# Optimization experiments

Measured on AMD Instinct MI355X. Metric: run time of the kernel, lower is better.

Reference implementation:

```python
import jax, jax.numpy as jnp
import numpy as np

N = 100000      # nodes
E = 1600000     # edges (avg degree 16)
D = 64          # feature dim


def setup_inputs() -> dict:
    key = jax.random.key(0)
    k1, k2, k3, k4 = jax.random.split(key, 4)
    x = jax.random.normal(k1, (N, D), dtype=jnp.float32)
    indices = jax.random.randint(k2, (E,), 0, N, dtype=jnp.int64)
    # valid CSR indptr: sorted, starts at 0, ends at E
    inner = jnp.sort(jax.random.randint(k3, (N - 1,), 0, E, dtype=jnp.int64))
    indptr = jnp.concatenate([
        jnp.zeros((1,), dtype=jnp.int64),
        inner,
        jnp.full((1,), E, dtype=jnp.int64),
    ])
    values = jax.random.normal(k4, (E,), dtype=jnp.float32)
    return {"x": x, "indptr": indptr, "indices": indices, "values": values}


def reference(x, indptr, indices, values):
    # CSR SpMM: out[i] = sum_{k in [indptr[i], indptr[i+1])} values[k] * x[indices[k]]
    num_edges = indices.shape[0]
    num_nodes = indptr.shape[0] - 1
    # recover row id of each edge from indptr (CSR row decompression)
    row = jnp.searchsorted(indptr, jnp.arange(num_edges, dtype=indptr.dtype), side='right') - 1
    gathered = values[:, None] * x[indices]            # [E, D] irregular gather
    out = jax.ops.segment_sum(gathered, row, num_segments=num_nodes)  # [N, D]
    return out
```

## Files before the change

kernel.cpp:

```cpp
#include <hip/hip_runtime.h>

#define DIM 64

__global__ __launch_bounds__(256) void spmm_quad_kernel(
    const float* __restrict__ x,
    const int*   __restrict__ indptr,
    const int*   __restrict__ indices,
    const float* __restrict__ values,
    float*       __restrict__ out,
    int n_nodes)
{
    const int row  = (int)((blockIdx.x * blockDim.x + threadIdx.x) >> 6);
    const int lane = (int)(threadIdx.x & 63);
    if (row >= n_nodes) return;

    const int start = indptr[row];
    const int end   = indptr[row + 1];
    const int g     = lane >> 4;
    const unsigned col4 = (unsigned)(lane & 15) << 2;

    float ax = 0.f, ay = 0.f, az = 0.f, aw = 0.f;

    if (start < end) {
        const int last = end - 1;
        for (int k = start; k < end; k += 16) {
            const int e0 = k +  0 + g;
            const int e1 = k +  4 + g;
            const int e2 = k +  8 + g;
            const int e3 = k + 12 + g;
            const int ce0 = e0 <= last ? e0 : last;
            const int ce1 = e1 <= last ? e1 : last;
            const int ce2 = e2 <= last ? e2 : last;
            const int ce3 = e3 <= last ? e3 : last;

            const int c0 = indices[ce0];
            const int c1 = indices[ce1];
            const int c2 = indices[ce2];
            const int c3 = indices[ce3];
            const float w0 = (e0 <= last) ? values[ce0] : 0.0f;
            const float w1 = (e1 <= last) ? values[ce1] : 0.0f;
            const float w2 = (e2 <= last) ? values[ce2] : 0.0f;
            const float w3 = (e3 <= last) ? values[ce3] : 0.0f;

            const float4 a0 = *(const float4*)(x + (((unsigned)c0) << 6) + col4);
            const float4 a1 = *(const float4*)(x + (((unsigned)c1) << 6) + col4);
            const float4 a2 = *(const float4*)(x + (((unsigned)c2) << 6) + col4);
            const float4 a3 = *(const float4*)(x + (((unsigned)c3) << 6) + col4);

            ax += w0 * a0.x; ay += w0 * a0.y; az += w0 * a0.z; aw += w0 * a0.w;
            ax += w1 * a1.x; ay += w1 * a1.y; az += w1 * a1.z; aw += w1 * a1.w;
            ax += w2 * a2.x; ay += w2 * a2.y; az += w2 * a2.z; aw += w2 * a2.w;
            ax += w3 * a3.x; ay += w3 * a3.y; az += w3 * a3.z; aw += w3 * a3.w;
        }
    }

    ax += __shfl_xor(ax, 16); ay += __shfl_xor(ay, 16);
    az += __shfl_xor(az, 16); aw += __shfl_xor(aw, 16);
    ax += __shfl_xor(ax, 32); ay += __shfl_xor(ay, 32);
    az += __shfl_xor(az, 32); aw += __shfl_xor(aw, 32);

    if (lane < 16) {
        float4 r; r.x = ax; r.y = ay; r.z = az; r.w = aw;
        *(float4*)(out + ((size_t)row << 6) + col4) = r;
    }
}

extern "C" void kernel_launch(void* const* d_in, const int* in_sizes, int n_in,
                              void* d_out, int out_size, void* d_ws, size_t ws_size,
                              hipStream_t stream) {
    const float* x       = (const float*)d_in[0];
    const int*   indptr  = (const int*)  d_in[1];
    const int*   indices = (const int*)  d_in[2];
    const float* values  = (const float*)d_in[3];
    float*       out     = (float*)d_out;

    const int n_nodes = in_sizes[1] - 1;

    const int threads = 256;
    const int rows_per_block = threads / 64;
    const int blocks = (n_nodes + rows_per_block - 1) / rows_per_block;

    spmm_quad_kernel<<<blocks, threads, 0, stream>>>(
        x, indptr, indices, values, out, n_nodes);
}
```

Baseline: 61.75 us.

## Convert x to fp16 in workspace and gather half-precision rows in SpMM

Adds a pre-pass kernel that converts the dense feature matrix to fp16 in the workspace. A new SpMM kernel then gathers 128-byte half rows with 8 lanes per edge and 8 edges per wave-step, accumulating in fp32. The aim is to halve the bytes moved by the irregular gather, at the cost of an extra conversion pass over x each call and a loss of precision in the inputs. If the workspace is too small it falls back to the original fp32 kernel.

```diff
diff --git a/kernel.cpp b/kernel.cpp
--- a/kernel.cpp
+++ b/kernel.cpp
@@ -1,6 +1,83 @@
 #include <hip/hip_runtime.h>
+#include <hip/hip_fp16.h>
 
 #define DIM 64
+
+__global__ __launch_bounds__(256) void cvt_half_kernel(
+    const float* __restrict__ x, __half* __restrict__ xh, int n4)
+{
+    int i = blockIdx.x * blockDim.x + threadIdx.x;
+    const int stride = gridDim.x * blockDim.x;
+    for (; i < n4; i += stride) {
+        const float4 v = ((const float4*)x)[i];
+        __half2 h0 = __floats2half2_rn(v.x, v.y);
+        __half2 h1 = __floats2half2_rn(v.z, v.w);
+        uint2 u;
+        u.x = *(const unsigned int*)&h0;
+        u.y = *(const unsigned int*)&h1;
+        ((uint2*)xh)[i] = u;
+    }
+}
+
+__global__ __launch_bounds__(256) void spmm_half_kernel(
+    const __half* __restrict__ xh,
+    const int*   __restrict__ indptr,
+    const int*   __restrict__ indices,
+    const float* __restrict__ values,
+    float*       __restrict__ out,
+    int n_nodes)
+{
+    const int row  = (int)((blockIdx.x * blockDim.x + threadIdx.x) >> 6);
+    const int lane = (int)(threadIdx.x & 63);
+    if (row >= n_nodes) return;
+    const int g = lane >> 3;
+    const int t = lane & 7;
+
+    const int start = indptr[row];
+    const int end   = indptr[row + 1];
+
+    float a0=0.f,a1=0.f,a2=0.f,a3=0.f,a4=0.f,a5=0.f,a6=0.f,a7=0.f;
+
+    if (start < end) {
+        const int last = end - 1;
+        for (int k = start; k < end; k += 16) {
+            const int e0 = k + g;
+            const int e1 = k + 8 + g;
+            const int ce0 = (e0 <= last) ? e0 : last;
+            const int ce1 = (e1 <= last) ? e1 : last;
+            const int c0 = indices[ce0];
+            const int c1 = indices[ce1];
+            const float w0 = (e0 <= last) ? values[ce0] : 0.0f;
+            const float w1 = (e1 <= last) ? values[ce1] : 0.0f;
+
+            const uint4 p0 = *(const uint4*)(xh + (((unsigned)c0) << 6) + (t << 3));
+            const uint4 p1 = *(const uint4*)(xh + (((unsigned)c1) << 6) + (t << 3));
+
+            float2 f;
+            f = __half22float2(*(const __half2*)&p0.x); a0 += w0*f.x; a1 += w0*f.y;
+            f = __half22float2(*(const __half2*)&p0.y); a2 += w0*f.x; a3 += w0*f.y;
+            f = __half22float2(*(const __half2*)&p0.z); a4 += w0*f.x; a5 += w0*f.y;
+            f = __half22float2(*(const __half2*)&p0.w); a6 += w0*f.x; a7 += w0*f.y;
+            f = __half22float2(*(const __half2*)&p1.x); a0 += w1*f.x; a1 += w1*f.y;
+            f = __half22float2(*(const __half2*)&p1.y); a2 += w1*f.x; a3 += w1*f.y;
+            f = __half22float2(*(const __half2*)&p1.z); a4 += w1*f.x; a5 += w1*f.y;
+            f = __half22float2(*(const __half2*)&p1.w); a6 += w1*f.x; a7 += w1*f.y;
+        }
+    }
+
+#define RED(m) a0+=__shfl_xor(a0,m); a1+=__shfl_xor(a1,m); a2+=__shfl_xor(a2,m); a3+=__shfl_xor(a3,m); \
+               a4+=__shfl_xor(a4,m); a5+=__shfl_xor(a5,m); a6+=__shfl_xor(a6,m); a7+=__shfl_xor(a7,m);
+    RED(8) RED(16) RED(32)
+#undef RED
+
+    if (lane < 8) {
+        float4 r0; r0.x=a0; r0.y=a1; r0.z=a2; r0.w=a3;
+        float4 r1; r1.x=a4; r1.y=a5; r1.z=a6; r1.w=a7;
+        float* dst = out + (((size_t)row) << 6) + (t << 3);
+        *(float4*)(dst)     = r0;
+        *(float4*)(dst + 4) = r1;
+    }
+}
 
 __global__ __launch_bounds__(256) void spmm_quad_kernel(
     const float* __restrict__ x,
@@ -24,29 +101,21 @@
     if (start < end) {
         const int last = end - 1;
         for (int k = start; k < end; k += 16) {
-            const int e0 = k +  0 + g;
-            const int e1 = k +  4 + g;
-            const int e2 = k +  8 + g;
-            const int e3 = k + 12 + g;
+            const int e0 = k +  0 + g, e1 = k + 4 + g, e2 = k + 8 + g, e3 = k + 12 + g;
             const int ce0 = e0 <= last ? e0 : last;
             const int ce1 = e1 <= last ? e1 : last;
             const int ce2 = e2 <= last ? e2 : last;
             const int ce3 = e3 <= last ? e3 : last;
-
-            const int c0 = indices[ce0];
-            const int c1 = indices[ce1];
-            const int c2 = indices[ce2];
-            const int c3 = indices[ce3];
+            const int c0 = indices[ce0], c1 = indices[ce1];
+            const int c2 = indices[ce2], c3 = indices[ce3];
             const float w0 = (e0 <= last) ? values[ce0] : 0.0f;
             const float w1 = (e1 <= last) ? values[ce1] : 0.0f;
             const float w2 = (e2 <= last) ? values[ce2] : 0.0f;
             const float w3 = (e3 <= last) ? values[ce3] : 0.0f;
-
             const float4 a0 = *(const float4*)(x + (((unsigned)c0) << 6) + col4);
             const float4 a1 = *(const float4*)(x + (((unsigned)c1) << 6) + col4);
             const float4 a2 = *(const float4*)(x + (((unsigned)c2) << 6) + col4);
             const float4 a3 = *(const float4*)(x + (((unsigned)c3) << 6) + col4);
-
             ax += w0 * a0.x; ay += w0 * a0.y; az += w0 * a0.z; aw += w0 * a0.w;
             ax += w1 * a1.x; ay += w1 * a1.y; az += w1 * a1.z; aw += w1 * a1.w;
             ax += w2 * a2.x; ay += w2 * a2.y; az += w2 * a2.z; aw += w2 * a2.w;
@@ -75,11 +144,21 @@
     float*       out     = (float*)d_out;
 
     const int n_nodes = in_sizes[1] - 1;
+    const int n_xelem = in_sizes[0];
 
     const int threads = 256;
     const int rows_per_block = threads / 64;
     const int blocks = (n_nodes + rows_per_block - 1) / rows_per_block;
 
-    spmm_quad_kernel<<<blocks, threads, 0, stream>>>(
-        x, indptr, indices, values, out, n_nodes);
+    const size_t needed = (size_t)n_xelem * sizeof(__half);
+    if (ws_size >= needed) {
+        __half* xh = (__half*)d_ws;
+        const int n4 = n_xelem / 4;
+        cvt_half_kernel<<<2048, 256, 0, stream>>>(x, xh, n4);
+        spmm_half_kernel<<<blocks, threads, 0, stream>>>(
+            xh, indptr, indices, values, out, n_nodes);
+    } else {
+        spmm_quad_kernel<<<blocks, threads, 0, stream>>>(
+            x, indptr, indices, values, out, n_nodes);
+    }
 }
```

New measurement: 53.18 us. -13.9%, faster.
